# Kernel optimization log

Hardware: AMD Instinct MI355X
Metric: run time of the kernel (lower is better)

## Reference

```python
import jax, jax.numpy as jnp
import numpy as np

LN_EPS = 1e-5

def _layer_norm(x, g, b):
    mu = jnp.mean(x, axis=-1, keepdims=True)
    var = jnp.mean(jnp.square(x - mu), axis=-1, keepdims=True)
    return g * (x - mu) * jax.lax.rsqrt(var + LN_EPS) + b

def setup_inputs() -> dict:
    key = jax.random.key(0)
    ks = jax.random.split(key, 12)
    N, E, D, V = 25000, 400000, 128, 16
    x = jax.random.normal(ks[0], (N, 3), dtype=jnp.float32)
    h = jax.random.normal(ks[1], (N, D), dtype=jnp.float32)
    edge_index = jax.random.randint(ks[2], (2, E), 0, N, dtype=jnp.int64)
    local_frames = jax.random.normal(ks[3], (N, 3, 3), dtype=jnp.float32)
    batch = jnp.zeros((N,), dtype=jnp.int64)
    v_prev = jax.random.normal(ks[4], (N, V, 3), dtype=jnp.float32)
    # vector_init params: Linear(D, 3V) -> LN -> SiLU -> Linear(3V, 3V) -> LN -> SiLU
    lim1 = np.sqrt(6.0 / (D + 3 * V))
    W1 = jax.random.uniform(ks[5], (3 * V, D), minval=-lim1, maxval=lim1, dtype=jnp.float32)
    b1 = jnp.zeros((3 * V,), jnp.float32)
    g1 = jnp.ones((3 * V,), jnp.float32); bb1 = jnp.zeros((3 * V,), jnp.float32)
    lim2 = np.sqrt(6.0 / (3 * V + 3 * V))
    W2 = jax.random.uniform(ks[6], (3 * V, 3 * V), minval=-lim2, maxval=lim2, dtype=jnp.float32)
    b2 = jnp.zeros((3 * V,), jnp.float32)
    g2 = jnp.ones((3 * V,), jnp.float32); bb2 = jnp.zeros((3 * V,), jnp.float32)
    # vector_interaction params: Linear(2D, 2V*V) -> LN -> Sigmoid
    limi = np.sqrt(6.0 / (2 * D + 2 * V * V))
    Wi = jax.random.uniform(ks[7], (2 * V * V, 2 * D), minval=-limi, maxval=limi, dtype=jnp.float32)
    bi = jnp.zeros((2 * V * V,), jnp.float32)
    gi = jnp.ones((2 * V * V,), jnp.float32); bbi = jnp.zeros((2 * V * V,), jnp.float32)
    return {"x": x, "h": h, "edge_index": edge_index, "local_frames": local_frames,
            "batch": batch, "v_prev": v_prev,
            "W1": W1, "b1": b1, "g1": g1, "bb1": bb1,
            "W2": W2, "b2": b2, "g2": g2, "bb2": bb2,
            "Wi": Wi, "bi": bi, "gi": gi, "bbi": bbi}

def reference(x, h, edge_index, local_frames, batch, v_prev,
              W1, b1, g1, bb1, W2, b2, g2, bb2, Wi, bi, gi, bbi):
    N = x.shape[0]
    V = v_prev.shape[1]  # vector_dim
    row, col = edge_index[0], edge_index[1]
    # vector_init: two Linear+LN+SiLU blocks -> [N, V, 3]
    t = jax.nn.silu(_layer_norm(h @ W1.T + b1, g1, bb1))
    t = jax.nn.silu(_layer_norm(t @ W2.T + b2, g2, bb2))
    vectors = t.reshape(N, V, 3)
    hi, hj = h[col], h[row]           # [E, D]
    vi, vj = vectors[col], vectors[row]  # [E, V, 3]
    Ri, Rj = local_frames[col], local_frames[row]  # [E, 3, 3]
    # R_rel = Ri^T @ Rj
    R_rel = jnp.einsum('eji,ejk->eik', Ri, Rj)
    vj_in_i = jnp.einsum('eij,ecj->eci', R_rel, vj)  # rotate sender vectors
    stacked_vectors = jnp.concatenate([vi, vj_in_i], axis=1)  # [E, 2V, 3]
    stacked_norms = jnp.concatenate([hi, hj], axis=-1)        # [E, 2D]
    w = jax.nn.sigmoid(_layer_norm(stacked_norms @ Wi.T + bi, gi, bbi))
    int_weights = w.reshape(-1, 2 * V, V)                     # [E, 2V, V]
    v_new = jnp.einsum('eko,ekc->eco', stacked_vectors, int_weights)  # [E, V, 3]
    v_out = jax.ops.segment_sum(v_new, col, num_segments=N)  # scatter-add on receiver
    return v_prev + v_out
```

## Files before the change

kernel.cpp:

```cpp
#include <hip/hip_runtime.h>


#define DD 128
#define VV 16
#define TV 48
#define NK 512

typedef __attribute__((ext_vector_type(8))) short short8;
typedef __attribute__((ext_vector_type(4))) float f32x4;

__device__ __forceinline__ unsigned short f2bf(float f){
    union{float f; unsigned u;} v; v.f = f;
    unsigned r = v.u + 0x7fffu + ((v.u >> 16) & 1u);
    return (unsigned short)(r >> 16);
}
__device__ __forceinline__ float bf2f(unsigned short h){
    union{unsigned u; float f;} v; v.u = ((unsigned)h) << 16; return v.f;
}
__device__ __forceinline__ float bf2f_hi(unsigned u){
    union{unsigned u; float f;} v; v.u = u & 0xffff0000u; return v.f;
}
__device__ __forceinline__ float bf2f_lo(unsigned u){
    union{unsigned u; float f;} v; v.u = u << 16; return v.f;
}
__device__ __forceinline__ void unpack8(uint4 q, float* d){
    d[0]=bf2f_lo(q.x); d[1]=bf2f_hi(q.x);
    d[2]=bf2f_lo(q.y); d[3]=bf2f_hi(q.y);
    d[4]=bf2f_lo(q.z); d[5]=bf2f_hi(q.z);
    d[6]=bf2f_lo(q.w); d[7]=bf2f_hi(q.w);
}
__device__ __forceinline__ float waveRedSum64(float v){
    #pragma unroll
    for (int off = 32; off > 0; off >>= 1) v += __shfl_xor(v, off, 64);
    return v;
}

__global__ void prep_k(const int* __restrict__ p, int nchk, int* __restrict__ flag,
                       int* __restrict__ cnt, int N){
    int i = blockIdx.x*blockDim.x + threadIdx.x;
    if (i < N) cnt[i] = 0;
    if (blockIdx.x == 0){
        __shared__ int s;
        if (threadIdx.x == 0) s = 0;
        __syncthreads();
        int nz = 0;
        for (int k = threadIdx.x; k < nchk; k += blockDim.x) nz |= (p[2*k+1] != 0);
        if (nz) atomicOr(&s, 1);
        __syncthreads();
        if (threadIdx.x == 0) *flag = s ? 0 : 1;
    }
}

__global__ void cvt_hist(const void* __restrict__ src, int* __restrict__ dst,
                         int* __restrict__ cnt, int n, int E,
                         const int* __restrict__ flag){
    int i = blockIdx.x*blockDim.x + threadIdx.x;
    if (i >= n) return;
    int v = (*flag) ? (int)((const long long*)src)[i] : ((const int*)src)[i];
    dst[i] = v;
    if (i >= E) atomicAdd(&cnt[v], 1);
}

__global__ __launch_bounds__(1024) void scan_k(const int* __restrict__ cnt,
        int* __restrict__ start, int* __restrict__ cursor, int N){
    __shared__ int wsum[16];
    __shared__ int woff[16];
    __shared__ int btot;
    __shared__ int carry;
    int tid = threadIdx.x;
    int lane = tid & 63, wid = tid >> 6;
    if (tid == 0) carry = 0;
    __syncthreads();
    for (int base = 0; base < N; base += 1024){
        int i = base + tid;
        int x = (i < N) ? cnt[i] : 0;
        int v = x;
        #pragma unroll
        for (int off = 1; off < 64; off <<= 1){
            int t = __shfl_up(v, off, 64);
            if (lane >= off) v += t;
        }
        if (lane == 63) wsum[wid] = v;
        __syncthreads();
        if (wid == 0 && lane < 16){
            int s = wsum[lane];
            int sv = s;
            #pragma unroll
            for (int off = 1; off < 16; off <<= 1){
                int t = __shfl_up(sv, off, 64);
                if (lane >= off) sv += t;
            }
            woff[lane] = sv - s;
            if (lane == 15) btot = sv;
        }
        __syncthreads();
        if (i < N){
            int excl = v - x + woff[wid] + carry;
            start[i] = excl;
            cursor[i] = excl;
        }
        __syncthreads();
        if (tid == 0) carry += btot;
        __syncthreads();
    }
    if (tid == 0) start[N] = carry;
}

__global__ void scatter_k(const int* __restrict__ idx, int* __restrict__ cursor,
                          int* __restrict__ elist, int E){
    int e = blockIdx.x*blockDim.x + threadIdx.x;
    if (e >= E) return;
    int col = idx[E + e], row = idx[e];
    int pos = atomicAdd(&cursor[col], 1);
    elist[pos] = row;
}

__global__ void build_wt(const float* __restrict__ Wi, const float* __restrict__ bi,
                         const float* __restrict__ gi, const float* __restrict__ bbi,
                         unsigned short* __restrict__ Wtb, float* __restrict__ bias_t,
                         float* __restrict__ gi_t, float* __restrict__ bbi_t){
    int j = blockIdx.x;
    int d = threadIdx.x;
    int half = j >> 9;
    int jj = j & 511;
    int c = jj >> 5, kk = jj & 31;
    int k = kk*16 + c;
    Wtb[(size_t)j*128 + d] = f2bf(Wi[k*256 + half*128 + d]);
    if (d == 0){
        bias_t[j] = half ? 0.0f : bi[k];
        if (!half){ gi_t[jj] = -gi[k]; bbi_t[jj] = -bbi[k]; }
    }
}

__global__ __launch_bounds__(256) void vinit(
        const float* __restrict__ h,
        const float* __restrict__ W1, const float* __restrict__ b1,
        const float* __restrict__ g1, const float* __restrict__ bb1,
        const float* __restrict__ W2, const float* __restrict__ b2,
        const float* __restrict__ g2, const float* __restrict__ bb2,
        const float* __restrict__ frames,
        float* __restrict__ vecs, float* __restrict__ gvec,
        unsigned short* __restrict__ hbh, unsigned short* __restrict__ hbl, int N){
    __shared__ float hs[4][DD];
    __shared__ float ts[4][TV];
    int w = threadIdx.x >> 6, l = threadIdx.x & 63;
    int n = blockIdx.x*4 + w;
    int nr = n < N ? n : N-1;
    float hv0 = h[(size_t)nr*DD + l];
    float hv1 = h[(size_t)nr*DD + 64 + l];
    hs[w][l]      = hv0;
    hs[w][l + 64] = hv1;
    if (n < N){
        unsigned short h0 = f2bf(hv0), h1 = f2bf(hv1);
        hbh[(size_t)n*DD + l]      = h0;
        hbh[(size_t)n*DD + 64 + l] = h1;
        hbl[(size_t)n*DD + l]      = f2bf(hv0 - bf2f(h0));
        hbl[(size_t)n*DD + 64 + l] = f2bf(hv1 - bf2f(h1));
    }
    __syncthreads();

    float o1 = 0.0f;
    if (l < TV){
        o1 = b1[l];
        const float* wr = W1 + l*DD;
        #pragma unroll
        for (int d = 0; d < DD; d += 4){
            float4 w4 = *(const float4*)(wr + d);
            o1 += hs[w][d]*w4.x + hs[w][d+1]*w4.y + hs[w][d+2]*w4.z + hs[w][d+3]*w4.w;
        }
    }
    float s  = waveRedSum64(l < TV ? o1 : 0.0f);
    float mu = s * (1.0f/TV);
    float dv = l < TV ? (o1 - mu) : 0.0f;
    float sq = waveRedSum64(dv*dv);
    float inv = rsqrtf(sq*(1.0f/TV) + 1e-5f);
    if (l < TV){
        float y = g1[l]*(dv*inv) + bb1[l];
        ts[w][l] = y / (1.0f + __expf(-y));
    }
    __syncthreads();

    float o2 = 0.0f;
    if (l < TV){
        o2 = b2[l];
        const float* wr = W2 + l*TV;
        #pragma unroll
        for (int j = 0; j < TV; j += 4){
            float4 w4 = *(const float4*)(wr + j);
            o2 += ts[w][j]*w4.x + ts[w][j+1]*w4.y + ts[w][j+2]*w4.z + ts[w][j+3]*w4.w;
        }
    }
    s  = waveRedSum64(l < TV ? o2 : 0.0f);
    mu = s * (1.0f/TV);
    dv = l < TV ? (o2 - mu) : 0.0f;
    sq = waveRedSum64(dv*dv);
    inv = rsqrtf(sq*(1.0f/TV) + 1e-5f);
    __syncthreads();
    if (l < TV){
        float y = g2[l]*(dv*inv) + bb2[l];
        float t2 = y / (1.0f + __expf(-y));
        if (n < N) vecs[(size_t)n*TV + l] = t2;
        ts[w][l] = t2;
    }
    __syncthreads();
    if (l < TV && n < N){
        int cc = l/3, oo = l%3;
        const float* R = frames + (size_t)n*9;
        float gv = R[oo*3+0]*ts[w][cc*3+0] + R[oo*3+1]*ts[w][cc*3+1] + R[oo*3+2]*ts[w][cc*3+2];
        gvec[(size_t)n*TV + l] = gv;
    }
}

__global__ __launch_bounds__(256) void gemm_mfma(
        const unsigned short* __restrict__ hbh, const unsigned short* __restrict__ hbl,
        const unsigned short* __restrict__ Wtb, const float* __restrict__ bias_t,
        unsigned short* __restrict__ P, int Np){
    int wv = threadIdx.x >> 6, l = threadIdx.x & 63;
    int lr = l & 15, g = l >> 4;
    int m0 = (blockIdx.y*4 + wv)*16;
    int n0 = blockIdx.x*256;

    f32x4 acc[16];
    #pragma unroll
    for (int nf = 0; nf < 16; nf++) acc[nf] = (f32x4){0.f,0.f,0.f,0.f};

    const unsigned short* arow_h = hbh + (size_t)(m0 + lr)*128;
    const unsigned short* arow_l = hbl + (size_t)(m0 + lr)*128;

    #pragma unroll
    for (int ks = 0; ks < 128; ks += 32){
        int kb = ks + 4*g;
        short8 ah, al;
        ((ushort4*)&ah)[0] = *(const ushort4*)(arow_h + kb);
        ((ushort4*)&ah)[1] = *(const ushort4*)(arow_h + kb + 16);
        ((ushort4*)&al)[0] = *(const ushort4*)(arow_l + kb);
        ((ushort4*)&al)[1] = *(const ushort4*)(arow_l + kb + 16);
        #pragma unroll
        for (int nf = 0; nf < 16; nf++){
            const unsigned short* brow = Wtb + (size_t)(n0 + nf*16 + lr)*128;
            short8 b;
            ((ushort4*)&b)[0] = *(const ushort4*)(brow + kb);
            ((ushort4*)&b)[1] = *(const ushort4*)(brow + kb + 16);
            acc[nf] = __builtin_amdgcn_mfma_f32_16x16x32_bf16(ah, b, acc[nf], 0, 0, 0);
            acc[nf] = __builtin_amdgcn_mfma_f32_16x16x32_bf16(al, b, acc[nf], 0, 0, 0);
        }
    }
    #pragma unroll
    for (int nf = 0; nf < 16; nf++){
        int col = n0 + nf*16 + lr;
        float bs = bias_t[col];
        #pragma unroll
        for (int r = 0; r < 4; r++){
            P[(size_t)(m0 + g*4 + r)*1024 + col] = f2bf(acc[nf][r] + bs);
        }
    }
}

__global__ __launch_bounds__(256) void node_k(
        const unsigned short* __restrict__ P, const float* __restrict__ vecs,
        const float* __restrict__ gvec, const float* __restrict__ frames,
        const int* __restrict__ start, const int* __restrict__ elist,
        const float* __restrict__ vprev, const float* __restrict__ gi_t,
        const float* __restrict__ bbi_t, float* __restrict__ out, int N){
    __shared__ float svs[4][4][100];
    int wv = threadIdx.x >> 6, ln = threadIdx.x & 63;
    int sub = ln >> 4, c = ln & 15;
    int n0 = blockIdx.x*4 + wv;
    int n = n0 < N ? n0 : N-1;

    {
        const float* vc = vecs + (size_t)n*TV + c*3;
        svs[wv][sub][c*3+0] = vc[0];
        svs[wv][sub][c*3+1] = vc[1];
        svs[wv][sub][c*3+2] = vc[2];
    }
    float R[9];
    #pragma unroll
    for (int i = 0; i < 9; i++) R[i] = frames[(size_t)n*9 + i];

    float pa[32];
    {
        const uint4* p4 = (const uint4*)(P + (size_t)n*1024 + c*32);
        #pragma unroll
        for (int q = 0; q < 4; q++) unpack8(p4[q], pa + 8*q);
    }
    int e0 = start[n], e1 = start[n+1];
    float a0 = 0.f, a1 = 0.f, a2 = 0.f;

    for (int t = e0 + sub; t < e1; t += 4){
        int row = elist[t];
        float l[32]; float s = 0.f, s2 = 0.f;
        {
            const uint4* p4 = (const uint4*)(P + (size_t)row*1024 + 512 + c*32);
            #pragma unroll
            for (int q = 0; q < 4; q++){
                float tmp[8]; unpack8(p4[q], tmp);
                #pragma unroll
                for (int r = 0; r < 8; r++){
                    float x = pa[8*q+r] + tmp[r];
                    l[8*q+r] = x;
                    s += x; s2 = fmaf(x, x, s2);
                }
            }
        }
        #pragma unroll
        for (int off = 1; off < 16; off <<= 1){
            s  += __shfl_xor(s,  off, 64);
            s2 += __shfl_xor(s2, off, 64);
        }
        float mu  = s * (1.0f/NK);
        float var = fmaf(-mu, mu, s2 * (1.0f/NK));
        float inv = rsqrtf(var + 1e-5f);

        {
            const float* gr = gvec + (size_t)row*TV + c*3;
            float g0 = gr[0], g1 = gr[1], g2 = gr[2];
            svs[wv][sub][48+c*3+0] = R[0]*g0 + R[3]*g1 + R[6]*g2;
            svs[wv][sub][48+c*3+1] = R[1]*g0 + R[4]*g1 + R[7]*g2;
            svs[wv][sub][48+c*3+2] = R[2]*g0 + R[5]*g1 + R[8]*g2;
        }
        {
            const float4* g4 = (const float4*)(gi_t  + c*32);
            const float4* b4 = (const float4*)(bbi_t + c*32);
            #pragma unroll
            for (int q = 0; q < 8; q++){
                float4 gg = g4[q], bb = b4[q];
                float gx[4] = {gg.x, gg.y, gg.z, gg.w};
                float bx[4] = {bb.x, bb.y, bb.z, bb.w};
                #pragma unroll
                for (int r = 0; r < 4; r++){
                    float z = (l[4*q+r] - mu) * inv;
                    float yn = fmaf(gx[r], z, bx[r]);
                    l[4*q+r] = 1.0f / (1.0f + __expf(yn));
                }
            }
        }
        {
            const float4* sv4 = (const float4*)&svs[wv][sub][0];
            #pragma unroll
            for (int q = 0; q < 24; q++){
                float4 x = sv4[q];
                {   const int e = 4*q+0, ch = e/3, o = e%3;
                    float p = x.x * l[ch];
                    if (o==0) a0 += p; else if (o==1) a1 += p; else a2 += p; }
                {   const int e = 4*q+1, ch = e/3, o = e%3;
                    float p = x.y * l[ch];
                    if (o==0) a0 += p; else if (o==1) a1 += p; else a2 += p; }
                {   const int e = 4*q+2, ch = e/3, o = e%3;
                    float p = x.z * l[ch];
                    if (o==0) a0 += p; else if (o==1) a1 += p; else a2 += p; }
                {   const int e = 4*q+3, ch = e/3, o = e%3;
                    float p = x.w * l[ch];
                    if (o==0) a0 += p; else if (o==1) a1 += p; else a2 += p; }
            }
        }
    }
    a0 += __shfl_xor(a0,16,64); a0 += __shfl_xor(a0,32,64);
    a1 += __shfl_xor(a1,16,64); a1 += __shfl_xor(a1,32,64);
    a2 += __shfl_xor(a2,16,64); a2 += __shfl_xor(a2,32,64);
    if (ln < 16 && n0 < N){
        size_t o = (size_t)n*TV + c*3;
        out[o+0] = vprev[o+0] + a0;
        out[o+1] = vprev[o+1] + a1;
        out[o+2] = vprev[o+2] + a2;
    }
}

extern "C" void kernel_launch(void* const* d_in, const int* in_sizes, int n_in,
                              void* d_out, int out_size, void* d_ws, size_t ws_size,
                              hipStream_t stream){
    const float* h      = (const float*)d_in[1];
    const void*  eidx   = d_in[2];
    const float* frames = (const float*)d_in[3];
    const float* vprev  = (const float*)d_in[5];
    const float* W1  = (const float*)d_in[6];
    const float* b1  = (const float*)d_in[7];
    const float* g1  = (const float*)d_in[8];
    const float* bb1 = (const float*)d_in[9];
    const float* W2  = (const float*)d_in[10];
    const float* b2  = (const float*)d_in[11];
    const float* g2  = (const float*)d_in[12];
    const float* bb2 = (const float*)d_in[13];
    const float* Wi  = (const float*)d_in[14];
    const float* bi  = (const float*)d_in[15];
    const float* gi  = (const float*)d_in[16];
    const float* bbi = (const float*)d_in[17];
    float* out = (float*)d_out;

    const int N = in_sizes[1] / DD;
    const int E = in_sizes[2] / 2;
    const int Np = ((N + 63) / 64) * 64;

    float* bias_t = (float*)d_ws;
    float* gi_t   = bias_t + 1024;
    float* bbi_t  = gi_t + 512;
    float* vecs   = bbi_t + 512;
    float* gvec   = vecs + (size_t)N*TV;
    unsigned short* Wtb = (unsigned short*)(gvec + (size_t)N*TV);
    unsigned short* hbh = Wtb + 1024*128;
    unsigned short* hbl = hbh + (size_t)Np*128;
    unsigned short* P   = hbl + (size_t)Np*128;
    int* idx32  = (int*)(P + (size_t)Np*1024);
    int* cnt    = idx32 + 2*(size_t)E;
    int* startp = cnt + N;
    int* cursor = startp + N + 1;
    int* elist  = cursor + N;
    int* dflag  = elist + E;

    int nchk = E < 4096 ? E : 4096;
    prep_k<<<(N + 255)/256, 256, 0, stream>>>((const int*)eidx, nchk, dflag, cnt, N);
    cvt_hist<<<(2*E + 255)/256, 256, 0, stream>>>(eidx, idx32, cnt, 2*E, E, dflag);
    build_wt<<<1024, 128, 0, stream>>>(Wi, bi, gi, bbi, Wtb, bias_t, gi_t, bbi_t);
    vinit<<<(N + 3)/4, 256, 0, stream>>>(h, W1, b1, g1, bb1, W2, b2, g2, bb2,
                                         frames, vecs, gvec, hbh, hbl, N);
    gemm_mfma<<<dim3(4, Np/64), 256, 0, stream>>>(hbh, hbl, Wtb, bias_t, P, Np);
    scan_k<<<1, 1024, 0, stream>>>(cnt, startp, cursor, N);
    scatter_k<<<(E + 255)/256, 256, 0, stream>>>(idx32, cursor, elist, E);
    node_k<<<(N + 3)/4, 256, 0, stream>>>(P, vecs, gvec, frames, startp, elist,
                                          vprev, gi_t, bbi_t, out, N);
    (void)ws_size; (void)n_in; (void)out_size;
}
```

Baseline: 673.2 us.

## Prefetch next edge's sender data and use native exp2/rcp in gather loop

The per-receiver edge loop now software-pipelines its gathers: the next edge's bf16 projection row and vector values are loaded into registers while the current edge is processed, hiding gather latency. The sigmoid now uses hardware exp2 and reciprocal intrinsics, with log2(e) folded into the precomputed LN gamma/beta. The two-pass mean/variance accumulation is split into two partial sums to shorten dependency chains. The cost is higher register pressure, which may lower occupancy, and slightly less accurate approximate reciprocal/exp.

```diff
diff --git a/kernel.cpp b/kernel.cpp
--- a/kernel.cpp
+++ b/kernel.cpp
@@ -5,9 +5,21 @@
 #define VV 16
 #define TV 48
 #define NK 512
+#define LOG2E 1.44269504088896340736f
 
 typedef __attribute__((ext_vector_type(8))) short short8;
 typedef __attribute__((ext_vector_type(4))) float f32x4;
+
+#if __has_builtin(__builtin_amdgcn_exp2f)
+#define EXP2F(x) __builtin_amdgcn_exp2f(x)
+#else
+#define EXP2F(x) exp2f(x)
+#endif
+#if __has_builtin(__builtin_amdgcn_rcpf)
+#define RCPF(x) __builtin_amdgcn_rcpf(x)
+#else
+#define RCPF(x) (1.0f/(x))
+#endif
 
 __device__ __forceinline__ unsigned short f2bf(float f){
     union{float f; unsigned u;} v; v.f = f;
@@ -128,7 +140,7 @@
     Wtb[(size_t)j*128 + d] = f2bf(Wi[k*256 + half*128 + d]);
     if (d == 0){
         bias_t[j] = half ? 0.0f : bi[k];
-        if (!half){ gi_t[jj] = -gi[k]; bbi_t[jj] = -bbi[k]; }
+        if (!half){ gi_t[jj] = -gi[k]*LOG2E; bbi_t[jj] = -bbi[k]*LOG2E; }
     }
 }
 
@@ -287,38 +299,52 @@
     int e0 = start[n], e1 = start[n+1];
     float a0 = 0.f, a1 = 0.f, a2 = 0.f;
 
-    for (int t = e0 + sub; t < e1; t += 4){
-        int row = elist[t];
-        float l[32]; float s = 0.f, s2 = 0.f;
+    int t = e0 + sub;
+    int rcur = elist[t < e1 ? t : 0];
+    uint4 pb0, pb1, pb2, pb3;
+    float gv0, gv1, gv2;
+    {
+        const uint4* p4 = (const uint4*)(P + (size_t)rcur*1024 + 512 + c*32);
+        pb0 = p4[0]; pb1 = p4[1]; pb2 = p4[2]; pb3 = p4[3];
+        const float* gr = gvec + (size_t)rcur*TV + c*3;
+        gv0 = gr[0]; gv1 = gr[1]; gv2 = gr[2];
+    }
+
+    for (; t < e1; t += 4){
+        int tn = t + 4;
+        int rnext = elist[tn < e1 ? tn : 0];
+        uint4 nb0, nb1, nb2, nb3;
+        float ng0, ng1, ng2;
         {
-            const uint4* p4 = (const uint4*)(P + (size_t)row*1024 + 512 + c*32);
-            #pragma unroll
-            for (int q = 0; q < 4; q++){
-                float tmp[8]; unpack8(p4[q], tmp);
-                #pragma unroll
-                for (int r = 0; r < 8; r++){
-                    float x = pa[8*q+r] + tmp[r];
-                    l[8*q+r] = x;
-                    s += x; s2 = fmaf(x, x, s2);
-                }
-            }
-        }
+            const uint4* p4 = (const uint4*)(P + (size_t)rnext*1024 + 512 + c*32);
+            nb0 = p4[0]; nb1 = p4[1]; nb2 = p4[2]; nb3 = p4[3];
+            const float* gr = gvec + (size_t)rnext*TV + c*3;
+            ng0 = gr[0]; ng1 = gr[1]; ng2 = gr[2];
+        }
+
+        float l[32];
+        unpack8(pb0, l+0); unpack8(pb1, l+8); unpack8(pb2, l+16); unpack8(pb3, l+24);
+        float sA = 0.f, sB = 0.f, qA = 0.f, qB = 0.f;
+        #pragma unroll
+        for (int i = 0; i < 16; i++){
+            float xa = pa[i]    + l[i];    l[i]    = xa; sA += xa; qA = fmaf(xa, xa, qA);
+            float xb = pa[16+i] + l[16+i]; l[16+i] = xb; sB += xb; qB = fmaf(xb, xb, qB);
+        }
+        float s = sA + sB, sq = qA + qB;
         #pragma unroll
         for (int off = 1; off < 16; off <<= 1){
             s  += __shfl_xor(s,  off, 64);
-            s2 += __shfl_xor(s2, off, 64);
+            sq += __shfl_xor(sq, off, 64);
         }
         float mu  = s * (1.0f/NK);
-        float var = fmaf(-mu, mu, s2 * (1.0f/NK));
+        float var = fmaf(-mu, mu, sq * (1.0f/NK));
         float inv = rsqrtf(var + 1e-5f);
-
-        {
-            const float* gr = gvec + (size_t)row*TV + c*3;
-            float g0 = gr[0], g1 = gr[1], g2 = gr[2];
-            svs[wv][sub][48+c*3+0] = R[0]*g0 + R[3]*g1 + R[6]*g2;
-            svs[wv][sub][48+c*3+1] = R[1]*g0 + R[4]*g1 + R[7]*g2;
-            svs[wv][sub][48+c*3+2] = R[2]*g0 + R[5]*g1 + R[8]*g2;
-        }
+        float nmi = -mu * inv;
+
+        svs[wv][sub][48+c*3+0] = R[0]*gv0 + R[3]*gv1 + R[6]*gv2;
+        svs[wv][sub][48+c*3+1] = R[1]*gv0 + R[4]*gv1 + R[7]*gv2;
+        svs[wv][sub][48+c*3+2] = R[2]*gv0 + R[5]*gv1 + R[8]*gv2;
+
         {
             const float4* g4 = (const float4*)(gi_t  + c*32);
             const float4* b4 = (const float4*)(bbi_t + c*32);
@@ -329,9 +355,9 @@
                 float bx[4] = {bb.x, bb.y, bb.z, bb.w};
                 #pragma unroll
                 for (int r = 0; r < 4; r++){
-                    float z = (l[4*q+r] - mu) * inv;
-                    float yn = fmaf(gx[r], z, bx[r]);
-                    l[4*q+r] = 1.0f / (1.0f + __expf(yn));
+                    float z   = fmaf(l[4*q+r], inv, nmi);
+                    float arg = fmaf(gx[r], z, bx[r]);
+                    l[4*q+r]  = RCPF(1.0f + EXP2F(arg));
                 }
             }
         }
@@ -354,6 +380,8 @@
                     if (o==0) a0 += p; else if (o==1) a1 += p; else a2 += p; }
             }
         }
+        pb0 = nb0; pb1 = nb1; pb2 = nb2; pb3 = nb3;
+        gv0 = ng0; gv1 = ng1; gv2 = ng2;
     }
     a0 += __shfl_xor(a0,16,64); a0 += __shfl_xor(a0,32,64);
     a1 += __shfl_xor(a1,16,64); a1 += __shfl_xor(a1,32,64);
```

After: 582.1 us. 13.5% less time.
